# Performance work log

Measured on AMD Instinct MI355X. Metric: run time of the kernel, lower is better.

The kernel has to match this reference:

```python
import jax, jax.numpy as jnp
import numpy as np

HID = 2048
NH = 16
NKV = 16
HD = HID // NH          # 128
ROPE_BASE = 100000.0
ROPE_SCALE = 4.0
B, L = 2, 2048
NEG = -1e9


def rope(x, offset=0):
    # x: [B, NH, L, HD]; half-split (rotate-half) RoPE with linear scaling
    Lx = x.shape[2]
    D = HD // 2
    pos = (jnp.arange(offset, offset + Lx, dtype=jnp.float32) / ROPE_SCALE)  # [L]
    freq = jnp.exp(-jnp.arange(D, dtype=jnp.float32) * (np.log(ROPE_BASE) / D))  # [D]
    m_theta = pos[:, None] * freq[None, :]          # [L, D]
    cos, sin = jnp.cos(m_theta), jnp.sin(m_theta)
    x1, x2 = x[..., :D], x[..., D:]
    rx1 = x1 * cos - x2 * sin
    rx2 = x1 * sin + x2 * cos
    return jnp.concatenate([rx1, rx2], axis=-1)


def setup_inputs() -> dict:
    key = jax.random.key(0)
    ks = jax.random.split(key, 5)
    x = jax.random.normal(ks[0], (B, L, HID), dtype=jnp.float32)
    # additive causal mask [1,1,L,L]
    mask = jnp.triu(jnp.full((L, L), NEG, dtype=jnp.float32), k=1)[None, None]
    Wq = jax.random.normal(ks[1], (HID, NH * HD), dtype=jnp.float32) * 0.02
    Wk = jax.random.normal(ks[2], (HID, NKV * HD), dtype=jnp.float32) * 0.02
    Wv = jax.random.normal(ks[3], (HID, NKV * HD), dtype=jnp.float32) * 0.02
    Wo = jax.random.normal(ks[4], (NH * HD, HID), dtype=jnp.float32) * 0.02
    return {"x": x, "mask": mask, "Wq": Wq, "Wk": Wk, "Wv": Wv, "Wo": Wo}


def reference(x, mask, Wq, Wk, Wv, Wo):
    b, l, _ = x.shape
    scale = HD ** -0.5
    q = (x @ Wq).reshape(b, l, NH, HD).transpose(0, 2, 1, 3)    # [B,NH,L,HD]
    k = (x @ Wk).reshape(b, l, NKV, HD).transpose(0, 2, 1, 3)
    v = (x @ Wv).reshape(b, l, NKV, HD).transpose(0, 2, 1, 3)
    rep = NH // NKV
    if rep > 1:
        k = jnp.repeat(k, rep, axis=1)
        v = jnp.repeat(v, rep, axis=1)
    q = rope(q)
    k = rope(k)
    scores = scale * jnp.einsum('bhqd,bhkd->bhqk', q, k)        # [B,NH,L,L]
    scores = scores + mask
    attn = jax.nn.softmax(scores, axis=-1)
    out = jnp.einsum('bhqk,bhkd->bhqd', attn, v)                # [B,NH,L,HD]
    out = out.transpose(0, 2, 1, 3).reshape(b, l, NH * HD)
    return out @ Wo
```

## Files before the change

kernel.cpp:

```cpp
#include <hip/hip_runtime.h>
#include <math.h>

#define BB   2
#define LL   2048
#define HIDD 2048
#define NHH  16
#define HDD  128
#define QKVN 6144
#define THR2 11.5416f

typedef unsigned short u16;
typedef float  f32x4 __attribute__((ext_vector_type(4)));
typedef __bf16 bf16x8 __attribute__((ext_vector_type(8)));

static __device__ __forceinline__ float exp2_fast(float x){
  return __builtin_amdgcn_exp2f(x);
}
static __device__ __forceinline__ u16 f2bf(float x){
  unsigned u = __float_as_uint(x);
  return (u16)((u + 0x7fffu + ((u >> 16) & 1u)) >> 16);
}
static __device__ __forceinline__ float bf2f(u16 b){
  return __uint_as_float(((unsigned)b) << 16);
}
static __device__ __forceinline__ void gl_lds16(const void* g, void* l){
  __builtin_amdgcn_global_load_lds(
      (__attribute__((address_space(1))) void*)(void*)g,
      (__attribute__((address_space(3))) void*)l,
      16, 0, 0);
}


__global__ void cvt_f32_bf16_k(const float* __restrict__ src, u16* __restrict__ dst, int n4){
  int i = blockIdx.x * blockDim.x + threadIdx.x;
  if (i >= n4) return;
  float4 v = ((const float4*)src)[i];
  ushort4 o;
  o.x = f2bf(v.x); o.y = f2bf(v.y); o.z = f2bf(v.z); o.w = f2bf(v.w);
  ((ushort4*)dst)[i] = o;
}

__global__ void transpose_cvt_k(const float* __restrict__ src, u16* __restrict__ dst, int R, int C){
  __shared__ float t[32][33];
  int c0 = blockIdx.x * 32, r0 = blockIdx.y * 32;
  int tx = threadIdx.x, ty = threadIdx.y;
  #pragma unroll
  for (int i = 0; i < 32; i += 8) t[ty + i][tx] = src[(size_t)(r0 + ty + i) * C + c0 + tx];
  __syncthreads();
  #pragma unroll
  for (int i = 0; i < 32; i += 8) dst[(size_t)(c0 + ty + i) * R + r0 + tx] = f2bf(t[tx][ty + i]);
}

__global__ void rope_k(u16* __restrict__ qkv){
  int idx = blockIdx.x * blockDim.x + threadIdx.x;
  int d   = idx & 63;
  int h   = (idx >> 6) & 15;
  int row = idx >> 10;
  int l   = row & (LL - 1);
  float fr = __expf(-(float)d * 0.17988946f);
  float th = (float)l * 0.25f * fr;
  float s, c;
  sincosf(th, &s, &c);
  size_t base = (size_t)row * QKVN + h * HDD + d;
  #pragma unroll
  for (int part = 0; part < 2; part++){
    float f = (part == 0) ? 0.12753375f : 1.0f;
    float x1 = bf2f(qkv[base]), x2 = bf2f(qkv[base + 64]);
    qkv[base]      = f2bf((x1 * c - x2 * s) * f);
    qkv[base + 64] = f2bf((x1 * s + x2 * c) * f);
    base += HIDD;
  }
}

__global__ void build_vt_k(const u16* __restrict__ qkv, u16* __restrict__ vt){
  __shared__ u16 t[32][33];
  int bh = blockIdx.z;
  int b = bh >> 4, h = bh & 15;
  const u16* src = qkv + (size_t)b * LL * QKVN + 2 * HIDD + h * HDD;
  u16* dst = vt + (size_t)bh * HDD * LL;
  int d0 = blockIdx.x * 32, l0 = blockIdx.y * 32;
  int tx = threadIdx.x, ty = threadIdx.y;
  #pragma unroll
  for (int i = 0; i < 32; i += 8) t[ty + i][tx] = src[(size_t)(l0 + ty + i) * QKVN + d0 + tx];
  __syncthreads();
  #pragma unroll
  for (int i = 0; i < 32; i += 8) dst[(size_t)(d0 + ty + i) * LL + l0 + tx] = t[tx][ty + i];
}


template<int OUT_BF16>
__global__ __launch_bounds__(256) void gemm_bt_k(
    const u16* __restrict__ A, const u16* __restrict__ Bt,
    void* __restrict__ Cout, int M, int N, int K)
{
  __shared__ __align__(16) u16 As[128 * 64];
  __shared__ __align__(16) u16 Bs[128 * 64];
  const int tid = threadIdx.x, lane = tid & 63, wv = tid >> 6;
  const int wr = wv >> 1, wc = wv & 1;
  const int m0 = blockIdx.y * 128, n0 = blockIdx.x * 128;
  const int rq = lane >> 4, cl = lane & 15;

  const f32x4 Z = {0.f, 0.f, 0.f, 0.f};
  f32x4 acc[4][4];
  #pragma unroll
  for (int m = 0; m < 4; m++)
    #pragma unroll
    for (int n = 0; n < 4; n++) acc[m][n] = Z;

  for (int kt = 0; kt < K; kt += 64){
    #pragma unroll
    for (int i = 0; i < 4; i++){
      int fb = (i * 4 + wv) * 64;
      int p  = (fb + lane) * 16;
      int r  = p >> 7;
      int cbs = (p & 127) ^ ((r & 7) << 4);
      gl_lds16(A  + (size_t)(m0 + r) * K + kt + (cbs >> 1), &As[fb * 8]);
      gl_lds16(Bt + (size_t)(n0 + r) * K + kt + (cbs >> 1), &Bs[fb * 8]);
    }
    __syncthreads();
    #pragma unroll
    for (int ks = 0; ks < 2; ks++){
      const int kb = ks * 64 + rq * 16;
      bf16x8 a[4], b[4];
      #pragma unroll
      for (int m = 0; m < 4; m++){
        int r = wr * 64 + m * 16 + cl;
        a[m] = *(const bf16x8*)((const char*)As + r * 128 + (kb ^ ((r & 7) << 4)));
      }
      #pragma unroll
      for (int n = 0; n < 4; n++){
        int r = wc * 64 + n * 16 + cl;
        b[n] = *(const bf16x8*)((const char*)Bs + r * 128 + (kb ^ ((r & 7) << 4)));
      }
      #pragma unroll
      for (int m = 0; m < 4; m++)
        #pragma unroll
        for (int n = 0; n < 4; n++)
          acc[m][n] = __builtin_amdgcn_mfma_f32_16x16x32_bf16(a[m], b[n], acc[m][n], 0, 0, 0);
    }
    __syncthreads();
  }

  #pragma unroll
  for (int m = 0; m < 4; m++){
    int gr0 = m0 + wr * 64 + m * 16 + rq * 4;
    #pragma unroll
    for (int n = 0; n < 4; n++){
      int gc = n0 + wc * 64 + n * 16 + cl;
      #pragma unroll
      for (int rr = 0; rr < 4; rr++){
        if (OUT_BF16) ((u16*)Cout)[(size_t)(gr0 + rr) * N + gc] = f2bf(acc[m][n][rr]);
        else          ((float*)Cout)[(size_t)(gr0 + rr) * N + gc] = acc[m][n][rr];
      }
    }
  }
}


#define STAGE_K(jj, bsel) do {                                                            \
  _Pragma("unroll")                                                                       \
  for (int i_ = 0; i_ < 2; i_++){                                                         \
    int fb_ = (i_ * 8 + wv) * 64;                                                         \
    int p_  = (fb_ + lane) * 16;                                                          \
    int r_ = p_ >> 8; int cb_ = (p_ & 255) ^ ((r_ & 7) << 4);                             \
    gl_lds16(qkv + (size_t)(b * LL + (jj) * 64 + r_) * QKVN + HIDD + h * HDD + (cb_ >> 1),\
             &Kb[bsel][fb_ * 8]);                                                         \
  }                                                                                       \
} while(0)

#define STAGE_V(jj) do {                                                                  \
  _Pragma("unroll")                                                                       \
  for (int i_ = 0; i_ < 2; i_++){                                                         \
    int fb_ = (i_ * 8 + wv) * 64;                                                         \
    int p_  = (fb_ + lane) * 16;                                                          \
    int r_ = p_ >> 7; int cb_ = (p_ & 127) ^ ((r_ & 7) << 4);                             \
    gl_lds16(vt + (size_t)(bh * HDD + r_) * LL + (jj) * 64 + (cb_ >> 1), &Vs[fb_ * 8]);   \
  }                                                                                       \
} while(0)

__global__ __launch_bounds__(512, 1) void attn_k(
    const u16* __restrict__ qkv, const u16* __restrict__ vt,
    u16* __restrict__ aout)
{
  __shared__ __align__(16) u16 Kb[2][64 * 128];
  __shared__ __align__(16) u16 Vs[128 * 64];
  const int tid = threadIdx.x, lane = tid & 63, wv = tid >> 6;
  const int bh = blockIdx.x;
  const int pr = blockIdx.y;
  const int b = bh >> 4, h = bh & 15;
  const int rq = lane >> 4, cl = lane & 15;

  bf16x8 ones;
  #pragma unroll
  for (int i = 0; i < 8; i++) ones[i] = (__bf16)1.0f;
  const f32x4 Z = {0.f, 0.f, 0.f, 0.f};

  int cur = 0;
  STAGE_K(0, 0);

  #pragma unroll
  for (int ph = 0; ph < 2; ph++){
    const int qt = ph ? pr : (15 - pr);
    const int nj = 2 * qt + 2;

    bf16x8 qf[4];
    {
      const u16* qb = qkv + (size_t)(b * LL + qt * 128 + wv * 16 + cl) * QKVN + h * HDD + rq * 8;
      #pragma unroll
      for (int ks = 0; ks < 4; ks++) qf[ks] = *(const bf16x8*)(qb + ks * 32);
    }

    f32x4 acco[8], accl;
    float mst[4];
    #pragma unroll
    for (int n = 0; n < 8; n++) acco[n] = Z;
    accl = Z;
    #pragma unroll
    for (int rr = 0; rr < 4; rr++) mst[rr] = -INFINITY;

    const int wrow_hi = qt * 128 + wv * 16 + 15;

    if (ph == 0) __syncthreads();

    for (int j = 0; j < nj; j++){
      if (j + 1 < nj)      STAGE_K(j + 1, cur ^ 1);
      else if (ph == 0)    STAGE_K(0,     cur ^ 1);
      STAGE_V(j);
      const bool act = (j * 64 <= wrow_hi);

      f32x4 sv[4];
      if (act){
        const char* KsC = (const char*)&Kb[cur][0];
        #pragma unroll
        for (int ct = 0; ct < 4; ct++) sv[ct] = Z;
        #pragma unroll
        for (int ks = 0; ks < 4; ks++){
          const int kb = ks * 64 + rq * 16;
          #pragma unroll
          for (int ct = 0; ct < 4; ct++){
            int r = ct * 16 + cl;
            bf16x8 bfr = *(const bf16x8*)(KsC + r * 256 + (kb ^ ((r & 7) << 4)));
            sv[ct] = __builtin_amdgcn_mfma_f32_16x16x32_bf16(qf[ks], bfr, sv[ct], 0, 0, 0);
          }
        }
      }

      __syncthreads();

      if (act){
        char* pbase = (char*)&Kb[cur][0] + wv * 2048;
        const bool msk = (j >= 2 * qt);

        float p4[4][4], lmx[4];
        #pragma unroll
        for (int rr = 0; rr < 4; rr++) lmx[rr] = -1e30f;
        const int qg = qt * 128 + wv * 16 + rq * 4;
        #pragma unroll
        for (int ct = 0; ct < 4; ct++){
          int col = j * 64 + ct * 16 + cl;
          #pragma unroll
          for (int rr = 0; rr < 4; rr++){
            float v = sv[ct][rr];
            if (msk && col > qg + rr) v = -1e30f;
            p4[ct][rr] = v;
            lmx[rr] = fmaxf(lmx[rr], v);
          }
        }
        float need = -1e30f;
        #pragma unroll
        for (int rr = 0; rr < 4; rr++) need = fmaxf(need, lmx[rr] - mst[rr]);
        if (__any(need > THR2)){
          float mx[4];
          #pragma unroll
          for (int rr = 0; rr < 4; rr++) mx[rr] = lmx[rr];
          #pragma unroll
          for (int off = 1; off < 16; off <<= 1)
            #pragma unroll
            for (int rr = 0; rr < 4; rr++)
              mx[rr] = fmaxf(mx[rr], __shfl_xor(mx[rr], off, 64));
          #pragma unroll
          for (int rr = 0; rr < 4; rr++){
            float mn  = fmaxf(mst[rr], mx[rr]);
            float fsc = exp2_fast(mst[rr] - mn);
            mst[rr] = mn;
            accl[rr] *= fsc;
            #pragma unroll
            for (int n = 0; n < 8; n++) acco[n][rr] *= fsc;
          }
        }
        #pragma unroll
        for (int ct = 0; ct < 4; ct++)
          #pragma unroll
          for (int rr = 0; rr < 4; rr++){
            float e = exp2_fast(p4[ct][rr] - mst[rr]);
            int wr = rq * 4 + rr;
            *(u16*)(pbase + wr * 128 + (((ct * 16 + cl) * 2) ^ ((wr & 7) << 4))) = f2bf(e);
          }

        const char* VsC = (const char*)Vs;
        #pragma unroll
        for (int ks = 0; ks < 2; ks++){
          const int kvb = ks * 64 + rq * 16;
          bf16x8 pa = *(const bf16x8*)(pbase + cl * 128 + (kvb ^ ((cl & 7) << 4)));
          accl = __builtin_amdgcn_mfma_f32_16x16x32_bf16(pa, ones, accl, 0, 0, 0);
          #pragma unroll
          for (int n = 0; n < 8; n++){
            int r = n * 16 + cl;
            bf16x8 bfr = *(const bf16x8*)(VsC + r * 128 + (kvb ^ ((r & 7) << 4)));
            acco[n] = __builtin_amdgcn_mfma_f32_16x16x32_bf16(pa, bfr, acco[n], 0, 0, 0);
          }
        }
      }

      __syncthreads();
      cur ^= 1;
    }

    #pragma unroll
    for (int rr = 0; rr < 4; rr++){
      float inv = 1.0f / accl[rr];
      size_t grow = (size_t)(b * LL + qt * 128 + wv * 16 + rq * 4 + rr);
      #pragma unroll
      for (int n = 0; n < 8; n++)
        aout[grow * HIDD + h * HDD + n * 16 + cl] = f2bf(acco[n][rr] * inv);
    }
  }
}


extern "C" void kernel_launch(void* const* d_in, const int* in_sizes, int n_in,
                              void* d_out, int out_size, void* d_ws, size_t ws_size,
                              hipStream_t stream)
{
  const float* x  = (const float*)d_in[0];
  const float* Wq = (const float*)d_in[2];
  const float* Wk = (const float*)d_in[3];
  const float* Wv = (const float*)d_in[4];
  const float* Wo = (const float*)d_in[5];
  float* out = (float*)d_out;

  if (ws_size < 134217728ull) return;

  char* ws = (char*)d_ws;
  u16* xb   = (u16*)(ws);
  u16* Wt   = (u16*)(ws + 16777216ull);
  u16* Wot  = (u16*)(ws + 41943040ull);
  u16* qkv  = (u16*)(ws + 50331648ull);
  u16* vt   = (u16*)(ws + 100663296ull);
  u16* aout = (u16*)(ws + 117440512ull);

  cvt_f32_bf16_k<<<2097152 / 256, 256, 0, stream>>>(x, xb, 2097152);
  dim3 tb(32, 8);
  transpose_cvt_k<<<dim3(64, 64), tb, 0, stream>>>(Wq, Wt,                   2048, 2048);
  transpose_cvt_k<<<dim3(64, 64), tb, 0, stream>>>(Wk, Wt + 2048 * 2048,     2048, 2048);
  transpose_cvt_k<<<dim3(64, 64), tb, 0, stream>>>(Wv, Wt + 2 * 2048 * 2048, 2048, 2048);
  transpose_cvt_k<<<dim3(64, 64), tb, 0, stream>>>(Wo, Wot,                  2048, 2048);

  gemm_bt_k<1><<<dim3(6144 / 128, 4096 / 128), 256, 0, stream>>>(xb, Wt, qkv, 4096, 6144, 2048);
  rope_k<<<4194304 / 256, 256, 0, stream>>>(qkv);
  build_vt_k<<<dim3(4, 64, 32), tb, 0, stream>>>(qkv, vt);

  attn_k<<<dim3(32, 8), 512, 0, stream>>>(qkv, vt, aout);

  gemm_bt_k<0><<<dim3(2048 / 128, 4096 / 128), 256, 0, stream>>>(aout, Wot, out, 4096, 2048, 2048);
}
```

Baseline: 290.4 us.

## Double-buffer GEMM LDS tiles with 128x256 blocks of 512 threads

Replaces the single-buffered 128x128 GEMM kernel with a 128x256-tile, 8-wave kernel. It prefetches two K-stages of A and B into double-buffered LDS through direct global-to-LDS loads, and waits on vmcnt so loads overlap MFMA compute. It also raises wave priority around the MFMA bursts. The costs are a larger LDS footprint (96 KB) and one block per CU, and the smaller grid, especially for the output projection, may reduce occupancy and load balance.

```diff
diff --git a/kernel.cpp b/kernel.cpp
--- a/kernel.cpp
+++ b/kernel.cpp
@@ -88,17 +88,36 @@
 }
 
 
+#define G2_STAGE(kt, bsel) do {                                                           \
+  _Pragma("unroll")                                                                       \
+  for (int i_ = 0; i_ < 2; i_++){                            \
+    int c_ = ((i_ * 8 + wv) * 64) + lane;                                                 \
+    int p_ = c_ * 16;                                                                     \
+    int r_ = p_ >> 7; int cb_ = (p_ & 127) ^ ((r_ & 7) << 4);                             \
+    gl_lds16(A + (size_t)(m0 + r_) * K + (kt) + (cb_ >> 1),                               \
+             &AB[bsel][((i_ * 8 + wv) * 64) * 8]);                                        \
+  }                                                                                       \
+  _Pragma("unroll")                                                                       \
+  for (int i_ = 0; i_ < 4; i_++){                            \
+    int c_ = ((i_ * 8 + wv) * 64) + lane;                                                 \
+    int p_ = c_ * 16;                                                                     \
+    int r_ = p_ >> 7; int cb_ = (p_ & 127) ^ ((r_ & 7) << 4);                             \
+    gl_lds16(Bt + (size_t)(n0 + r_) * K + (kt) + (cb_ >> 1),                              \
+             &AB[bsel][8192 + ((i_ * 8 + wv) * 64) * 8]);                                 \
+  }                                                                                       \
+} while(0)
+
 template<int OUT_BF16>
-__global__ __launch_bounds__(256) void gemm_bt_k(
+__global__ __launch_bounds__(512, 1) void gemm_bt2_k(
     const u16* __restrict__ A, const u16* __restrict__ Bt,
     void* __restrict__ Cout, int M, int N, int K)
 {
-  __shared__ __align__(16) u16 As[128 * 64];
-  __shared__ __align__(16) u16 Bs[128 * 64];
+  __shared__ __align__(16) u16 AB[2][24576];
   const int tid = threadIdx.x, lane = tid & 63, wv = tid >> 6;
-  const int wr = wv >> 1, wc = wv & 1;
-  const int m0 = blockIdx.y * 128, n0 = blockIdx.x * 128;
+  const int wr = wv >> 2, wc = wv & 3;
+  const int m0 = blockIdx.y * 128, n0 = blockIdx.x * 256;
   const int rq = lane >> 4, cl = lane & 15;
+  const int NT = K >> 6;
 
   const f32x4 Z = {0.f, 0.f, 0.f, 0.f};
   f32x4 acc[4][4];
@@ -107,17 +126,17 @@
     #pragma unroll
     for (int n = 0; n < 4; n++) acc[m][n] = Z;
 
-  for (int kt = 0; kt < K; kt += 64){
-    #pragma unroll
-    for (int i = 0; i < 4; i++){
-      int fb = (i * 4 + wv) * 64;
-      int p  = (fb + lane) * 16;
-      int r  = p >> 7;
-      int cbs = (p & 127) ^ ((r & 7) << 4);
-      gl_lds16(A  + (size_t)(m0 + r) * K + kt + (cbs >> 1), &As[fb * 8]);
-      gl_lds16(Bt + (size_t)(n0 + r) * K + kt + (cbs >> 1), &Bs[fb * 8]);
-    }
-    __syncthreads();
+  G2_STAGE(0, 0);
+  G2_STAGE(64, 1);
+  asm volatile("s_waitcnt vmcnt(6)");
+  __builtin_amdgcn_sched_barrier(0);
+  __builtin_amdgcn_s_barrier();
+
+  int cur = 0;
+  for (int t = 0; t < NT; t++){
+    const char* As_ = (const char*)&AB[cur][0];
+    const char* Bs_ = (const char*)&AB[cur][8192];
+
     #pragma unroll
     for (int ks = 0; ks < 2; ks++){
       const int kb = ks * 64 + rq * 16;
@@ -125,20 +144,34 @@
       #pragma unroll
       for (int m = 0; m < 4; m++){
         int r = wr * 64 + m * 16 + cl;
-        a[m] = *(const bf16x8*)((const char*)As + r * 128 + (kb ^ ((r & 7) << 4)));
+        a[m] = *(const bf16x8*)(As_ + r * 128 + (kb ^ ((r & 7) << 4)));
       }
       #pragma unroll
       for (int n = 0; n < 4; n++){
         int r = wc * 64 + n * 16 + cl;
-        b[n] = *(const bf16x8*)((const char*)Bs + r * 128 + (kb ^ ((r & 7) << 4)));
-      }
+        b[n] = *(const bf16x8*)(Bs_ + r * 128 + (kb ^ ((r & 7) << 4)));
+      }
+      __builtin_amdgcn_s_setprio(1);
       #pragma unroll
       for (int m = 0; m < 4; m++)
         #pragma unroll
         for (int n = 0; n < 4; n++)
           acc[m][n] = __builtin_amdgcn_mfma_f32_16x16x32_bf16(a[m], b[n], acc[m][n], 0, 0, 0);
-    }
-    __syncthreads();
+      __builtin_amdgcn_s_setprio(0);
+    }
+
+    __builtin_amdgcn_sched_barrier(0);
+    __builtin_amdgcn_s_barrier();
+
+    if (t + 2 < NT){
+      G2_STAGE((t + 2) * 64, cur);
+      asm volatile("s_waitcnt vmcnt(6)");
+    } else {
+      asm volatile("s_waitcnt vmcnt(0)");
+    }
+    __builtin_amdgcn_sched_barrier(0);
+    __builtin_amdgcn_s_barrier();
+    cur ^= 1;
   }
 
   #pragma unroll
@@ -356,11 +389,11 @@
   transpose_cvt_k<<<dim3(64, 64), tb, 0, stream>>>(Wv, Wt + 2 * 2048 * 2048, 2048, 2048);
   transpose_cvt_k<<<dim3(64, 64), tb, 0, stream>>>(Wo, Wot,                  2048, 2048);
 
-  gemm_bt_k<1><<<dim3(6144 / 128, 4096 / 128), 256, 0, stream>>>(xb, Wt, qkv, 4096, 6144, 2048);
+  gemm_bt2_k<1><<<dim3(6144 / 256, 4096 / 128), 512, 0, stream>>>(xb, Wt, qkv, 4096, 6144, 2048);
   rope_k<<<4194304 / 256, 256, 0, stream>>>(qkv);
   build_vt_k<<<dim3(4, 64, 32), tb, 0, stream>>>(qkv, vt);
 
   attn_k<<<dim3(32, 8), 512, 0, stream>>>(qkv, vt, aout);
 
-  gemm_bt_k<0><<<dim3(2048 / 128, 4096 / 128), 256, 0, stream>>>(aout, Wot, out, 4096, 2048, 2048);
-}
+  gemm_bt2_k<0><<<dim3(2048 / 256, 4096 / 128), 512, 0, stream>>>(aout, Wot, out, 4096, 2048, 2048);
+}
```

Result: faster. 279.2 us (-3.9%).
